# Optimization experiments

Hardware: AMD Instinct MI355X
Metric: run time of the kernel (lower is better)

## Reference

```python
import jax, jax.numpy as jnp
import numpy as np
from jax import lax

MODEL_DIM = 384
KERNEL = 15
PAD = (KERNEL - 1) // 2
BATCH = 4096


def fake_quant(x, bits):
    """Per-tensor symmetric fake quantization with straight-through estimator.
    scale = max|x| / qmax, q = clip(round(x/scale), qmin, qmax), dq = q*scale.
    """
    qmax = float(2 ** (bits - 1) - 1)
    qmin = -float(2 ** (bits - 1))
    scale = jnp.maximum(jnp.max(jnp.abs(x)) / qmax, jnp.asarray(1e-8, x.dtype))
    dq = jnp.clip(jnp.round(x / scale), qmin, qmax) * scale
    return x + lax.stop_gradient(dq - x)  # STE: identity gradient


def setup_inputs() -> dict:
    key = jax.random.key(0)
    k = jax.random.split(key, 7)
    image = jax.random.normal(k[0], (BATCH, 28, 28), dtype=jnp.float32)
    # LinearQuant(28 -> model_dim)
    W1 = jax.random.normal(k[1], (MODEL_DIM, 28), dtype=jnp.float32) * (1.0 / np.sqrt(28))
    b1 = jax.random.normal(k[2], (MODEL_DIM,), dtype=jnp.float32) * 0.01
    # depthwise Conv1DQuant(model_dim, model_dim, K, groups=model_dim): weight [C_out, 1, K]
    Wc = jax.random.normal(k[3], (MODEL_DIM, 1, KERNEL), dtype=jnp.float32) * (1.0 / np.sqrt(KERNEL))
    bc = jax.random.normal(k[4], (MODEL_DIM,), dtype=jnp.float32) * 0.01
    # LinearQuant(28*model_dim -> 10)
    Wf = jax.random.normal(k[5], (10, 28 * MODEL_DIM), dtype=jnp.float32) * (1.0 / np.sqrt(28 * MODEL_DIM))
    bf = jax.random.normal(k[6], (10,), dtype=jnp.float32) * 0.01
    return {"image": image, "W1": W1, "b1": b1, "Wc": Wc, "bc": bc, "Wf": Wf, "bf": bf}


def reference(image, W1, b1, Wc, bc, Wf, bf):
    inp = image.reshape(-1, 28, 28)
    # linear_1 with 8-bit activation fake-quant in and 3-bit weight fake-quant
    x = fake_quant(inp, 8)
    lin = jnp.einsum('blf,of->blo', x, fake_quant(W1, 3)) + b1  # [B,28,model_dim]
    out1 = jnp.tanh(fake_quant(lin, 8))
    # depthwise conv1d over length 28, channels model_dim
    xc = jnp.transpose(fake_quant(out1, 8), (0, 2, 1))  # [B,C,L]
    conv = lax.conv_general_dilated(
        xc, fake_quant(Wc, 3), window_strides=(1,), padding=[(PAD, PAD)],
        dimension_numbers=('NCH', 'OIH', 'NCH'), feature_group_count=MODEL_DIM)
    conv = conv + bc[None, :, None]                      # [B,C,L]
    conv = jnp.transpose(conv, (0, 2, 1))                # [B,L,C]
    out2 = jnp.tanh(fake_quant(conv, 8)).reshape(-1, MODEL_DIM * 28)
    # final linear
    logits = fake_quant(out2, 8) @ fake_quant(Wf, 3).T + bf  # [B,10]
    return fake_quant(logits, 8)
```

## Files before the change

kernel.cpp:

```cpp
#include <hip/hip_runtime.h>

#define BATCH 4096
#define MD 384
#define KW 15
#define LSEQ 28
#define FIN 28
#define NX (BATCH*LSEQ*FIN)
#define NROWS (BATCH*LSEQ)

#define B_SCF  0
#define B_LUT1 256
#define B_LUT2 512
#define B_PT0  1024
#define B_PT1  33792
#define B_PT2  50176
#define B_PTL  66560
#define B_W1B  74752
#define B_WCQ  99328
#define B_WFB  105472
#define B_LG   277504
#define B_XQB  441344
#define B_CWG  7781376

typedef __bf16 bf16x8 __attribute__((ext_vector_type(8)));
typedef float f32x4 __attribute__((ext_vector_type(4)));
typedef int i32x4 __attribute__((ext_vector_type(4)));

#if __has_builtin(__builtin_amdgcn_sdot4)
#define SDOT4(a,b,c) __builtin_amdgcn_sdot4((a),(b),(c),false)
#else
__device__ __forceinline__ int SDOT4(int a,int b,int c){
  c += ((a<<24)>>24)*((b<<24)>>24);
  c += ((a<<16)>>24)*((b<<16)>>24);
  c += ((a<<8)>>24)*((b<<8)>>24);
  c += (a>>24)*(b>>24);
  return c;
}
#endif

#if __has_builtin(__builtin_amdgcn_alignbyte)
#define ALIGNB(hi,lo,s) __builtin_amdgcn_alignbyte((hi),(lo),(s))
#else
#define ALIGNB(hi,lo,s) ((int)(((unsigned)(lo)>>(8*(s)))|((unsigned)(hi)<<(32-8*(s)))))
#endif

__device__ __forceinline__ unsigned short f2bf(float f){
  return (unsigned short)(__float_as_uint(f)>>16);
}
__device__ __forceinline__ unsigned lut_bperm(int iw,int lutw){
  int res=__builtin_amdgcn_ds_bpermute(iw,lutw);
  return ((unsigned)res>>(8*(iw&3)))&0xFFu;
}

__device__ __forceinline__ void blkStore4(float m0,float m1,float m2,float m3,float4* dst){
  #pragma unroll
  for(int off=32;off;off>>=1){
    m0=fmaxf(m0,__shfl_xor(m0,off,64));
    m1=fmaxf(m1,__shfl_xor(m1,off,64));
    m2=fmaxf(m2,__shfl_xor(m2,off,64));
    m3=fmaxf(m3,__shfl_xor(m3,off,64));
  }
  __shared__ float sm[4][4];
  int wid=threadIdx.x>>6;
  if((threadIdx.x&63)==0){sm[wid][0]=m0;sm[wid][1]=m1;sm[wid][2]=m2;sm[wid][3]=m3;}
  __syncthreads();
  if(threadIdx.x==0){
    for(int i=1;i<4;i++){
      m0=fmaxf(m0,sm[i][0]);m1=fmaxf(m1,sm[i][1]);
      m2=fmaxf(m2,sm[i][2]);m3=fmaxf(m3,sm[i][3]);
    }
    *dst=make_float4(m0,m1,m2,m3);
  }
}

__device__ __forceinline__ void blkStoreMM(float mn,float mx,float2* dst){
  #pragma unroll
  for(int off=32;off;off>>=1){
    mn=fminf(mn,__shfl_xor(mn,off,64));
    mx=fmaxf(mx,__shfl_xor(mx,off,64));
  }
  __shared__ float smn[8],smx[8];
  int wid=threadIdx.x>>6, nw=blockDim.x>>6;
  if((threadIdx.x&63)==0){smn[wid]=mn;smx[wid]=mx;}
  __syncthreads();
  if(threadIdx.x==0){
    for(int i=1;i<nw;i++){mn=fminf(mn,smn[i]);mx=fmaxf(mx,smx[i]);}
    *dst=make_float2(mn,mx);
  }
}

__global__ __launch_bounds__(256)
void k_maxabs_in(const float* __restrict__ img,const float* __restrict__ W1,
                 const float* __restrict__ Wc,const float* __restrict__ Wf,
                 float4* __restrict__ pt0){
  float m0=0.f,m1=0.f,m2=0.f,m3=0.f;
  const int N4=NX/4;
  const int NW1=MD*FIN, NWC=MD*KW, NWF=10*MD*LSEQ;
  const int total=N4+NW1+NWC+NWF;
  const float4* img4=(const float4*)img;
  for(int i=blockIdx.x*blockDim.x+threadIdx.x;i<total;i+=gridDim.x*blockDim.x){
    if(i<N4){
      float4 v=img4[i];
      m0=fmaxf(m0,fmaxf(fmaxf(fabsf(v.x),fabsf(v.y)),fmaxf(fabsf(v.z),fabsf(v.w))));
    }
    else if(i<N4+NW1) m1=fmaxf(m1,fabsf(W1[i-N4]));
    else if(i<N4+NW1+NWC) m2=fmaxf(m2,fabsf(Wc[i-N4-NW1]));
    else m3=fmaxf(m3,fabsf(Wf[i-N4-NW1-NWC]));
  }
  blkStore4(m0,m1,m2,m3,&pt0[blockIdx.x]);
}

__global__ __launch_bounds__(256)
void k_red0(const float4* __restrict__ pt,float* __restrict__ scf){
  int t=threadIdx.x;
  float m0=0.f,m1=0.f,m2=0.f,m3=0.f;
  for(int i=t;i<2048;i+=256){
    float4 v=pt[i];
    m0=fmaxf(m0,v.x);m1=fmaxf(m1,v.y);m2=fmaxf(m2,v.z);m3=fmaxf(m3,v.w);
  }
  #pragma unroll
  for(int off=32;off;off>>=1){
    m0=fmaxf(m0,__shfl_xor(m0,off,64));
    m1=fmaxf(m1,__shfl_xor(m1,off,64));
    m2=fmaxf(m2,__shfl_xor(m2,off,64));
    m3=fmaxf(m3,__shfl_xor(m3,off,64));
  }
  __shared__ float sm[4][4];
  int wid=t>>6;
  if((t&63)==0){sm[wid][0]=m0;sm[wid][1]=m1;sm[wid][2]=m2;sm[wid][3]=m3;}
  __syncthreads();
  if(t==0){
    for(int i=1;i<4;i++){
      m0=fmaxf(m0,sm[i][0]);m1=fmaxf(m1,sm[i][1]);
      m2=fmaxf(m2,sm[i][2]);m3=fmaxf(m3,sm[i][3]);
    }
    scf[0]=fmaxf(m0/127.f,1e-8f);
    scf[1]=fmaxf(m1/3.f,1e-8f);
    scf[2]=fmaxf(m2/3.f,1e-8f);
    scf[3]=fmaxf(m3/3.f,1e-8f);
  }
}

__global__ __launch_bounds__(256)
void k_redmm(const float2* __restrict__ pt,int n,float* __restrict__ scf,
             int preIdx,int outIdx,char* __restrict__ lutg){
  int t=threadIdx.x;
  float mn=1e30f,mx=-1e30f;
  for(int i=t;i<n;i+=256){
    float2 v=pt[i];
    mn=fminf(mn,v.x); mx=fmaxf(mx,v.y);
  }
  #pragma unroll
  for(int off=32;off;off>>=1){
    mn=fminf(mn,__shfl_xor(mn,off,64));
    mx=fmaxf(mx,__shfl_xor(mx,off,64));
  }
  __shared__ float smn[4],smx[4];
  __shared__ float bs,bso;
  int wid=t>>6;
  if((t&63)==0){smn[wid]=mn;smx[wid]=mx;}
  __syncthreads();
  if(t==0){
    for(int i=1;i<4;i++){mn=fminf(mn,smn[i]);mx=fmaxf(mx,smx[i]);}
    float ma=fmaxf(fabsf(mn),fabsf(mx));
    float s=fmaxf(ma/127.f,1e-8f);
    float a1=fabsf(fminf(fmaxf(rintf(mn/s),-128.f),127.f)*s);
    float a2=fabsf(fminf(fmaxf(rintf(mx/s),-128.f),127.f)*s);
    float so=fmaxf(tanhf(fmaxf(a1,a2))/127.f,1e-8f);
    scf[preIdx]=s; scf[outIdx]=so;
    bs=s; bso=so;
  }
  __syncthreads();
  float d=(float)(t-128)*bs;
  lutg[t]=(char)(int)fminf(fmaxf(rintf(tanhf(d)/bso),-128.f),127.f);
}

__global__ __launch_bounds__(256)
void k_prep(const float* __restrict__ img,const float* __restrict__ W1,
            const float* __restrict__ Wc,const float* __restrict__ Wf,
            const float* __restrict__ scf,char* __restrict__ wsb){
  float s_img=scf[0], s_w1=scf[1], s_wc=scf[2], s_wf=scf[3];
  float inv_img=1.f/s_img;
  unsigned short* xqb=(unsigned short*)(wsb+B_XQB);
  unsigned short* w1b=(unsigned short*)(wsb+B_W1B);
  char* wcpk=wsb+B_WCQ;
  char* wfb=wsb+B_WFB;
  const int T0=NROWS*32;
  const int T1=T0+MD*32;
  const int T2=T1+MD*16;
  const int T3=T2+10*10752;
  for(int i=blockIdx.x*blockDim.x+threadIdx.x;i<T3;i+=gridDim.x*blockDim.x){
    if(i<T0){
      int row=i>>5, cc=i&31;
      float q = cc<FIN ? fminf(fmaxf(rintf(img[row*FIN+cc]*inv_img),-128.f),127.f) : 0.f;
      xqb[i]=f2bf(q);
    } else if(i<T1){
      int j=i-T0; int o=j>>5, cc=j&31;
      float q = cc<FIN ? fminf(fmaxf(rintf(W1[o*FIN+cc]/s_w1),-4.f),3.f) : 0.f;
      w1b[j]=f2bf(q);
    } else if(i<T2){
      int j=i-T1; int c=j>>4, k=j&15;
      char q=0;
      if(k<KW) q=(char)(int)fminf(fmaxf(rintf(Wc[c*KW+k]/s_wc),-4.f),3.f);
      wcpk[j]=q;
    } else {
      int j=i-T2;
      int n=j/10752, r=j-n*10752;
      int c=r/28, l=r-c*28;
      wfb[j]=(char)(int)fminf(fmaxf(rintf(Wf[n*10752+l*MD+c]/s_wf),-4.f),3.f);
    }
  }
}

#define CWS 29
#define DWS 2692
template<int MODE>
__global__ __launch_bounds__(512)
void k_fused(const unsigned short* __restrict__ xqb,const unsigned short* __restrict__ w1b,
             const float* __restrict__ b1,const float* __restrict__ scf,
             const char* __restrict__ lut1g,const char* __restrict__ lut2g,
             const char* __restrict__ wcpk,const float* __restrict__ bc,
             const char* __restrict__ wfb,const float* __restrict__ bfv,
             int* __restrict__ cwg,
             float2* __restrict__ ptmm,float* __restrict__ lg,
             float* __restrict__ ptl){
  __shared__ int ldsI[MD*CWS];
  __shared__ int psumN[8][10][4];
  int t=threadIdx.x, wid=t>>6, lane=t&63, l4=lane>>4, l15=lane&15;

  bf16x8 bfr[3]; float b1v[3]; bf16x8 af[7];
  if constexpr(MODE<2){
    const int* src=(const int*)w1b;
    for(int i=t;i<6144;i+=512) ldsI[i]=src[i];
    __syncthreads();
    unsigned short* Wlds=(unsigned short*)ldsI;
    #pragma unroll
    for(int ni=0;ni<3;ni++){
      int o=(wid*3+ni)*16+l15;
      bfr[ni]=*(const bf16x8*)&Wlds[o*32+l4*8];
      b1v[ni]=b1[o];
    }
    int r0=blockIdx.x*112;
    #pragma unroll
    for(int mt=0;mt<7;mt++)
      af[mt]=*(const bf16x8*)&xqb[(size_t)(r0+mt*16+l15)*32+l4*8];
  } else {
    const int4* src=(const int4*)(cwg+(size_t)blockIdx.x*10752);
    for(int jj=t;jj<2688;jj+=512){
      int4 v=src[jj];
      int j=jj*4, o=j/28, idx=j-o*28, base=o*CWS+idx;
      ldsI[base]=v.x; ldsI[base+1]=v.y; ldsI[base+2]=v.z; ldsI[base+3]=v.w;
    }
  }

  float sg=scf[0]*scf[1];
  float sgi=sg, b1s[3]={0.f,0.f,0.f};
  int lutA_w=0,lutB_w=0;
  float ck1=1.f,inv_cv=1.f,sfac=1.f,gsc=1.f;
  if constexpr(MODE>=1){
    sfac=scf[5]*scf[2];
  }
  if constexpr(MODE==1){
    float inv_lin=1.f/scf[4];
    sgi=sg*inv_lin;
    #pragma unroll
    for(int ni=0;ni<3;ni++) b1s[ni]=fmaf(b1v[ni],inv_lin,128.f);
    lutA_w=((const int*)lut1g)[lane];
  }
  if constexpr(MODE==2){
    inv_cv=1.f/scf[6];
    ck1=sfac*inv_cv;
    gsc=scf[3]*scf[7];
    lutB_w=((const int*)lut2g)[lane];
  }
  if constexpr(MODE>=1) __syncthreads();

  if constexpr(MODE<2){
    f32x4 zero={0.f,0.f,0.f,0.f};
    float mnn[3]={1e30f,1e30f,1e30f},mxx[3]={-1e30f,-1e30f,-1e30f};
    #pragma unroll
    for(int ni=0;ni<3;ni++){
      int o=(wid*3+ni)*16+l15;
      #pragma unroll
      for(int mt=0;mt<7;mt++){
        f32x4 acc=__builtin_amdgcn_mfma_f32_16x16x32_bf16(af[mt],bfr[ni],zero,0,0,0);
        if constexpr(MODE==0){
          #pragma unroll
          for(int r=0;r<4;r++){
            mnn[ni]=fminf(mnn[ni],acc[r]); mxx[ni]=fmaxf(mxx[ni],acc[r]);
          }
        } else {
          unsigned w=0;
          #pragma unroll
          for(int r=0;r<4;r++){
            float x=fmaf(acc[r],sgi,b1s[ni]);
            int iw=(int)__builtin_amdgcn_fmed3f(rintf(x),0.f,255.f);
            w|=lut_bperm(iw,lutA_w)<<(8*r);
          }
          ldsI[o*CWS+mt*4+l4]=(int)w;
        }
      }
    }
    if constexpr(MODE==0){
      float mn=1e30f,mx=-1e30f;
      #pragma unroll
      for(int ni=0;ni<3;ni++){
        mn=fminf(mn,fmaf(mnn[ni],sg,b1v[ni]));
        mx=fmaxf(mx,fmaf(mxx[ni],sg,b1v[ni]));
      }
      blkStoreMM(mn,mx,&ptmm[blockIdx.x]);
      return;
    }
    __syncthreads();
    {
      int4* dst=(int4*)(cwg+(size_t)blockIdx.x*10752);
      for(int jj=t;jj<2688;jj+=512){
        int j=jj*4, o=j/28, idx=j-o*28, base=o*CWS+idx;
        int4 v; v.x=ldsI[base]; v.y=ldsI[base+1]; v.z=ldsI[base+2]; v.w=ldsI[base+3];
        dst[jj]=v;
      }
    }
  }

  int oww[3][7];
  float mnc=1e30f,mxc=-1e30f;
  #pragma unroll
  for(int rr=0;rr<3;rr++){
    int j=t+rr*512;
    int s=j/384, c=j-s*384;
    i32x4 wq=*(const i32x4*)(wcpk+(size_t)c*16);
    float cbias=bc[c];
    float cq2=0.f;
    if constexpr(MODE==2) cq2=fmaf(cbias,inv_cv,128.f);
    int ext[11];
    ext[0]=0; ext[1]=0; ext[9]=0; ext[10]=0;
    #pragma unroll
    for(int i=0;i<7;i++) ext[2+i]=ldsI[c*CWS+s*7+i];
    int imn=0x7FFFFFFF,imx=0x80000000;
    #pragma unroll
    for(int l=0;l<LSEQ;l++){
      const int eb=l+1, bi=eb>>2, sh=eb&3;
      int A0,A1,A2,A3;
      if(sh==0){A0=ext[bi];A1=ext[bi+1];A2=ext[bi+2];A3=ext[bi+3];}
      else{
        A0=ALIGNB(ext[bi+1],ext[bi],sh);
        A1=ALIGNB(ext[bi+2],ext[bi+1],sh);
        A2=ALIGNB(ext[bi+3],ext[bi+2],sh);
        A3=ALIGNB(ext[bi+4],ext[bi+3],sh);
      }
      int idot=SDOT4(A0,wq[0],SDOT4(A1,wq[1],SDOT4(A2,wq[2],SDOT4(A3,wq[3],0))));
      if constexpr(MODE==1){
        imn=min(imn,idot); imx=max(imx,idot);
      } else {
        float x=fmaf((float)idot,ck1,cq2);
        int iw=(int)__builtin_amdgcn_fmed3f(rintf(x),0.f,255.f);
        unsigned q2=lut_bperm(iw,lutB_w);
        if((l&3)==0) oww[rr][l>>2]=(int)q2;
        else oww[rr][l>>2]|=(int)(q2<<(8*(l&3)));
      }
    }
    if constexpr(MODE==1){
      mnc=fminf(mnc,fmaf((float)imn,sfac,cbias));
      mxc=fmaxf(mxc,fmaf((float)imx,sfac,cbias));
    }
  }
  if constexpr(MODE==1){
    blkStoreMM(mnc,mxc,&ptmm[blockIdx.x]);
    return;
  }

  __syncthreads();
  #pragma unroll
  for(int rr=0;rr<3;rr++){
    int j=t+rr*512;
    int s=j/384, c=j-s*384;
    #pragma unroll
    for(int i=0;i<7;i++) ldsI[s*DWS+c*7+i]=oww[rr][i];
  }
  __syncthreads();

  {
    i32x4 acc={0,0,0,0};
    const char* ldsB=(const char*)ldsI;
    for(int kb=wid;kb<168;kb+=8){
      i32x4 a=*(const i32x4*)(ldsB+(size_t)(l15&3)*(DWS*4)+kb*64+l4*16);
      i32x4 b=*(const i32x4*)(wfb+(size_t)l15*10752+kb*64+l4*16);
      acc=__builtin_amdgcn_mfma_i32_16x16x64_i8(a,b,acc,0,0,0);
    }
    if(l4==0&&l15<10){
      #pragma unroll
      for(int r=0;r<4;r++) psumN[wid][l15][r]=acc[r];
    }
  }
  __syncthreads();
  float m=0.f;
  if(t<40){
    int s=t/10, o=t-s*10;
    int sum=0;
    #pragma unroll
    for(int w=0;w<8;w++) sum+=psumN[w][o][s];
    float v=fmaf((float)sum,gsc,bfv[o]);
    lg[(blockIdx.x*4+s)*10+o]=v;
    m=fabsf(v);
  }
  if(t<64){
    #pragma unroll
    for(int off=32;off;off>>=1) m=fmaxf(m,__shfl_xor(m,off,64));
    if(t==0) ptl[blockIdx.x]=m;
  }
}

__global__ __launch_bounds__(256)
void k_final(const float* __restrict__ lg,const float* __restrict__ ptl,
             float* __restrict__ out){
  int t=threadIdx.x;
  float m=0.f;
  for(int i=t;i<1024;i+=256) m=fmaxf(m,ptl[i]);
  #pragma unroll
  for(int off=32;off;off>>=1) m=fmaxf(m,__shfl_xor(m,off,64));
  __shared__ float sm[4];
  __shared__ float sv;
  int wid=t>>6;
  if((t&63)==0) sm[wid]=m;
  __syncthreads();
  if(t==0){
    for(int k=1;k<4;k++) m=fmaxf(m,sm[k]);
    sv=fmaxf(m/127.f,1e-8f);
  }
  __syncthreads();
  float s=sv;
  int i=blockIdx.x*256+t;
  out[i]=fminf(fmaxf(rintf(lg[i]/s),-128.f),127.f)*s;
}

extern "C" void kernel_launch(void* const* d_in, const int* in_sizes, int n_in,
                              void* d_out, int out_size, void* d_ws, size_t ws_size,
                              hipStream_t stream){
  const float* img=(const float*)d_in[0];
  const float* W1 =(const float*)d_in[1];
  const float* b1 =(const float*)d_in[2];
  const float* Wc =(const float*)d_in[3];
  const float* bc =(const float*)d_in[4];
  const float* Wf =(const float*)d_in[5];
  const float* bf =(const float*)d_in[6];
  float* out=(float*)d_out;
  char* wsb=(char*)d_ws;
  float* scf=(float*)(wsb+B_SCF);
  float4* pt0=(float4*)(wsb+B_PT0);
  float2* pt1=(float2*)(wsb+B_PT1);
  float2* pt2=(float2*)(wsb+B_PT2);
  float* ptl=(float*)(wsb+B_PTL);
  float* lg=(float*)(wsb+B_LG);
  int* cwg=(int*)(wsb+B_CWG);
  const unsigned short* xqb=(const unsigned short*)(wsb+B_XQB);
  const unsigned short* w1b=(const unsigned short*)(wsb+B_W1B);
  const char* wcpk=wsb+B_WCQ;
  const char* wfb=wsb+B_WFB;

  k_maxabs_in<<<2048,256,0,stream>>>(img,W1,Wc,Wf,pt0);
  k_red0<<<1,256,0,stream>>>(pt0,scf);
  k_prep<<<4096,256,0,stream>>>(img,W1,Wc,Wf,scf,wsb);
  k_fused<0><<<1024,512,0,stream>>>(xqb,w1b,b1,scf,nullptr,nullptr,wcpk,bc,wfb,bf,cwg,pt1,nullptr,nullptr);
  k_redmm<<<1,256,0,stream>>>(pt1,1024,scf,4,5,wsb+B_LUT1);
  k_fused<1><<<1024,512,0,stream>>>(xqb,w1b,b1,scf,wsb+B_LUT1,nullptr,wcpk,bc,wfb,bf,cwg,pt2,nullptr,nullptr);
  k_redmm<<<1,256,0,stream>>>(pt2,1024,scf,6,7,wsb+B_LUT2);
  k_fused<2><<<1024,512,0,stream>>>(xqb,w1b,b1,scf,wsb+B_LUT1,wsb+B_LUT2,wcpk,bc,wfb,bf,cwg,nullptr,lg,ptl);
  k_final<<<160,256,0,stream>>>(lg,ptl,out);
}
```

Baseline: 104.8 us.

## Replace MFMA final linear with in-place LDS writes and per-wave sdot4 reduction

The packed conv outputs are now written back in place into the existing LDS layout right after each channel/segment is computed. This drops the extra barrier and the transposed DWS-strided relayout. The final 10-output linear no longer uses a 16x16x64 int8 MFMA, which wasted 6 of 16 columns and 12 of 16 rows. Instead each wave computes one or two output neurons with SDOT4 over LDS plus coalesced weight reads, then reduces with wave shuffles. The risk is lower compute density, plus LDS bank conflicts from the strided c*29 addressing. Waves 2-7 idle on the second pass.

```diff
diff --git a/kernel.cpp b/kernel.cpp
--- a/kernel.cpp
+++ b/kernel.cpp
@@ -213,7 +213,6 @@
 }
 
 #define CWS 29
-#define DWS 2692
 template<int MODE>
 __global__ __launch_bounds__(512)
 void k_fused(const unsigned short* __restrict__ xqb,const unsigned short* __restrict__ w1b,
@@ -225,7 +224,6 @@
              float2* __restrict__ ptmm,float* __restrict__ lg,
              float* __restrict__ ptl){
   __shared__ int ldsI[MD*CWS];
-  __shared__ int psumN[8][10][4];
   int t=threadIdx.x, wid=t>>6, lane=t&63, l4=lane>>4, l15=lane&15;
 
   bf16x8 bfr[3]; float b1v[3]; bf16x8 af[7];
@@ -322,7 +320,6 @@
     }
   }
 
-  int oww[3][7];
   float mnc=1e30f,mxc=-1e30f;
   #pragma unroll
   for(int rr=0;rr<3;rr++){
@@ -337,6 +334,7 @@
     #pragma unroll
     for(int i=0;i<7;i++) ext[2+i]=ldsI[c*CWS+s*7+i];
     int imn=0x7FFFFFFF,imx=0x80000000;
+    unsigned oww[7];
     #pragma unroll
     for(int l=0;l<LSEQ;l++){
       const int eb=l+1, bi=eb>>2, sh=eb&3;
@@ -355,13 +353,16 @@
         float x=fmaf((float)idot,ck1,cq2);
         int iw=(int)__builtin_amdgcn_fmed3f(rintf(x),0.f,255.f);
         unsigned q2=lut_bperm(iw,lutB_w);
-        if((l&3)==0) oww[rr][l>>2]=(int)q2;
-        else oww[rr][l>>2]|=(int)(q2<<(8*(l&3)));
+        if((l&3)==0) oww[l>>2]=q2;
+        else oww[l>>2]|=q2<<(8*(l&3));
       }
     }
     if constexpr(MODE==1){
       mnc=fminf(mnc,fmaf((float)imn,sfac,cbias));
       mxc=fmaxf(mxc,fmaf((float)imx,sfac,cbias));
+    } else {
+      #pragma unroll
+      for(int i=0;i<7;i++) ldsI[c*CWS+s*7+i]=(int)oww[i];
     }
   }
   if constexpr(MODE==1){
@@ -369,44 +370,59 @@
     return;
   }
 
-  __syncthreads();
-  #pragma unroll
-  for(int rr=0;rr<3;rr++){
-    int j=t+rr*512;
-    int s=j/384, c=j-s*384;
-    #pragma unroll
-    for(int i=0;i<7;i++) ldsI[s*DWS+c*7+i]=oww[rr][i];
-  }
-  __syncthreads();
-
-  {
-    i32x4 acc={0,0,0,0};
-    const char* ldsB=(const char*)ldsI;
-    for(int kb=wid;kb<168;kb+=8){
-      i32x4 a=*(const i32x4*)(ldsB+(size_t)(l15&3)*(DWS*4)+kb*64+l4*16);
-      i32x4 b=*(const i32x4*)(wfb+(size_t)l15*10752+kb*64+l4*16);
-      acc=__builtin_amdgcn_mfma_i32_16x16x64_i8(a,b,acc,0,0,0);
-    }
-    if(l4==0&&l15<10){
+  if constexpr(MODE==2){
+    __shared__ float lgout[40];
+    __shared__ float lgmax[16];
+    __syncthreads();
+    const int* wfw=(const int*)wfb;
+    int c0=(lane*37)>>8;
+    int i0=lane-c0*7;
+    #pragma unroll
+    for(int p=0;p<2;p++){
+      int ow=wid+p*8;
+      int a0=0,a1=0,a2=0,a3=0;
+      if(ow<10){
+        int c=c0,i=i0;
+        const int* wrow=wfw+ow*2688;
+        #pragma unroll 6
+        for(int it=0;it<42;it++){
+          int base=c*CWS+i;
+          int wv=wrow[lane+it*64];
+          a0=SDOT4(ldsI[base],wv,a0);
+          a1=SDOT4(ldsI[base+7],wv,a1);
+          a2=SDOT4(ldsI[base+14],wv,a2);
+          a3=SDOT4(ldsI[base+21],wv,a3);
+          i+=1; c+=9; if(i>=7){i-=7;c+=1;}
+        }
+        #pragma unroll
+        for(int off=32;off;off>>=1){
+          a0+=__shfl_xor(a0,off,64);
+          a1+=__shfl_xor(a1,off,64);
+          a2+=__shfl_xor(a2,off,64);
+          a3+=__shfl_xor(a3,off,64);
+        }
+      }
+      if(lane==0){
+        float mm=0.f;
+        if(ow<10){
+          float v0=fmaf((float)a0,gsc,bfv[ow]);
+          float v1=fmaf((float)a1,gsc,bfv[ow]);
+          float v2=fmaf((float)a2,gsc,bfv[ow]);
+          float v3=fmaf((float)a3,gsc,bfv[ow]);
+          lgout[ow]=v0; lgout[10+ow]=v1; lgout[20+ow]=v2; lgout[30+ow]=v3;
+          mm=fmaxf(fmaxf(fabsf(v0),fabsf(v1)),fmaxf(fabsf(v2),fabsf(v3)));
+        }
+        lgmax[wid+p*8]=mm;
+      }
+    }
+    __syncthreads();
+    if(t<40) lg[(size_t)blockIdx.x*40+t]=lgout[t];
+    if(t<64){
+      float m=(t<16)?lgmax[t]:0.f;
       #pragma unroll
-      for(int r=0;r<4;r++) psumN[wid][l15][r]=acc[r];
-    }
-  }
-  __syncthreads();
-  float m=0.f;
-  if(t<40){
-    int s=t/10, o=t-s*10;
-    int sum=0;
-    #pragma unroll
-    for(int w=0;w<8;w++) sum+=psumN[w][o][s];
-    float v=fmaf((float)sum,gsc,bfv[o]);
-    lg[(blockIdx.x*4+s)*10+o]=v;
-    m=fabsf(v);
-  }
-  if(t<64){
-    #pragma unroll
-    for(int off=32;off;off>>=1) m=fmaxf(m,__shfl_xor(m,off,64));
-    if(t==0) ptl[blockIdx.x]=m;
+      for(int off=8;off;off>>=1) m=fmaxf(m,__shfl_xor(m,off,64));
+      if(t==0) ptl[blockIdx.x]=m;
+    }
   }
 }
 
```

Result: slower. 111.8 us (+6.7%).
